# Optimization experiments

Hardware: AMD Instinct MI355X
Metric: run time of the kernel (lower is better)

The kernel has to match this reference:

```python
import jax, jax.numpy as jnp
import numpy as np

B = 131072
OBS = 64
H = 512
LAT = 512
DPC = 32  # dim_per_component -> 16 components of size 32
LN_EPS = 1e-6  # flax nn.LayerNorm default


def _variance_scaling_uniform(key, shape, scale=1.0):
    # variance_scaling(scale, 'fan_avg', 'uniform')
    fan_in, fan_out = shape[0], shape[1]
    fan_avg = (fan_in + fan_out) / 2.0
    limit = np.sqrt(3.0 * scale / fan_avg)
    return jax.random.uniform(key, shape, jnp.float32, -limit, limit)


def setup_inputs() -> dict:
    key = jax.random.key(0)
    ks = jax.random.split(key, 8)
    inp = {
        'observations': jax.random.normal(ks[0], (B, OBS), jnp.float32),
        'goals': jax.random.normal(ks[1], (B, OBS), jnp.float32),
        'W0': _variance_scaling_uniform(ks[2], (OBS, H)),
        'b0': jnp.zeros((H,), jnp.float32),
        'ln0_s': jnp.ones((H,), jnp.float32),
        'ln0_b': jnp.zeros((H,), jnp.float32),
        'W1': _variance_scaling_uniform(ks[3], (H, H)),
        'b1': jnp.zeros((H,), jnp.float32),
        'ln1_s': jnp.ones((H,), jnp.float32),
        'ln1_b': jnp.zeros((H,), jnp.float32),
        'W2': _variance_scaling_uniform(ks[4], (H, H)),
        'b2': jnp.zeros((H,), jnp.float32),
        'ln2_s': jnp.ones((H,), jnp.float32),
        'ln2_b': jnp.zeros((H,), jnp.float32),
        'W3': _variance_scaling_uniform(ks[5], (H, LAT)),
        'b3': jnp.zeros((LAT,), jnp.float32),
        'alpha': jnp.zeros((), jnp.float32),
    }
    return inp


def _layer_norm(x, scale, bias):
    m = x.mean(axis=-1, keepdims=True)
    v = ((x - m) ** 2).mean(axis=-1, keepdims=True)
    return (x - m) / jnp.sqrt(v + LN_EPS) * scale + bias


def _phi(x, W0, b0, ln0_s, ln0_b, W1, b1, ln1_s, ln1_b, W2, b2, ln2_s, ln2_b, W3, b3):
    # LayerNormMLP with activate_final=False: gelu+LN after every layer except last
    x = _layer_norm(jax.nn.gelu(x @ W0 + b0), ln0_s, ln0_b)
    x = _layer_norm(jax.nn.gelu(x @ W1 + b1), ln1_s, ln1_b)
    x = _layer_norm(jax.nn.gelu(x @ W2 + b2), ln2_s, ln2_b)
    return x @ W3 + b3


def _iqe(phi_s, phi_g, alpha):
    # reshape [B, LAT] -> [B, n_components, DPC]
    x = phi_s.reshape(*phi_s.shape[:-1], -1, DPC)
    y = phi_g.reshape(*phi_g.shape[:-1], -1, DPC)
    valid = x < y
    xy = jnp.concatenate(jnp.broadcast_arrays(x, y), axis=-1)  # [B, C, 2*DPC]
    ixy = jnp.argsort(xy, axis=-1)
    sxy = jnp.take_along_axis(xy, ixy, axis=-1)
    neg_inc = jnp.take_along_axis(valid, ixy % DPC, axis=-1) * jnp.where(ixy < DPC, -1, 1)
    neg_inp = jnp.cumsum(neg_inc, axis=-1)
    neg_f = -1.0 * (neg_inp < 0)
    neg_incf = jnp.concatenate([neg_f[..., :1], neg_f[..., 1:] - neg_f[..., :-1]], axis=-1)
    components = (sxy * neg_incf).sum(axis=-1)  # [B, C]
    a = jax.nn.sigmoid(alpha)
    return a * components.mean(axis=-1) + (1.0 - a) * components.max(axis=-1)


def reference(observations, goals, W0, b0, ln0_s, ln0_b, W1, b1, ln1_s, ln1_b,
              W2, b2, ln2_s, ln2_b, W3, b3, alpha):
    params = (W0, b0, ln0_s, ln0_b, W1, b1, ln1_s, ln1_b, W2, b2, ln2_s, ln2_b, W3, b3)
    phi_s = _phi(observations, *params)
    phi_g = _phi(goals, *params)
    return _iqe(phi_s, phi_g, alpha)
```

## Files before the change

### kernel.cpp

```cpp
#include <hip/hip_runtime.h>
#include <hip/hip_bf16.h>
#include <hip/hip_fp16.h>

typedef unsigned short u16;
typedef unsigned int u32;
typedef __attribute__((ext_vector_type(8))) _Float16 f16x8;
typedef __attribute__((ext_vector_type(4))) float f32x4;

#define ROWS 32
#define SSTR 520
#define RSTR 20
#define NEG_INF (-3.0e38f)

__device__ __forceinline__ float bf2f(u16 b) {
  union { u32 u; float f; } c; c.u = ((u32)b) << 16; return c.f;
}
__device__ __forceinline__ u16 f2bf(float f) {
  union { float f; u32 u; } c; c.f = f;
  u32 r = c.u + 0x7FFFu + ((c.u >> 16) & 1u);
  return (u16)(r >> 16);
}
__device__ __forceinline__ float gelu_tanh(float x) {
  float u = 0.7978845608028654f * (x + 0.044715f * x * x * x);
  float e = __expf(2.f * u);
  float t = 1.f - 2.f / (e + 1.f);
  return 0.5f * x * (1.f + t);
}
__device__ __forceinline__ float ldp(const void* p, int i, int f32) {
  return f32 ? ((const float*)p)[i] : bf2f(((const u16*)p)[i]);
}
__device__ __forceinline__ f16x8 load8(const void* base, long off, int f32) {
  f16x8 r;
  if (f32) {
    const float4* p = (const float4*)((const float*)base + off);
    float4 a = p[0], b = p[1];
    r[0] = (_Float16)a.x; r[1] = (_Float16)a.y; r[2] = (_Float16)a.z; r[3] = (_Float16)a.w;
    r[4] = (_Float16)b.x; r[5] = (_Float16)b.y; r[6] = (_Float16)b.z; r[7] = (_Float16)b.w;
  } else {
    const u16* p = (const u16*)base + off;
#pragma unroll
    for (int i = 0; i < 8; ++i) r[i] = (_Float16)bf2f(p[i]);
  }
  return r;
}

__global__ void detect_dtype(const u16* __restrict__ obs, int* flag) {
  int l = threadIdx.x;
  float v = fabsf(bf2f(obs[2 * l]));
  if (v != v) v = 1e30f;
#pragma unroll
  for (int m = 1; m <= 32; m <<= 1) v = fmaxf(v, __shfl_xor(v, m, 64));
  if (l == 0) *flag = (v > 1000.0f) ? 1 : 0;
}

__global__ void pack_frag(const void* __restrict__ src, u16* __restrict__ dst,
                          const int* __restrict__ flag, int total,
                          int fshift, int cishift, int tmask) {
  int id = blockIdx.x * 256 + threadIdx.x;
  if (id >= total) return;
  int j = id & 7;
  int lane = (id >> 3) & 63;
  int fi = id >> 9;
  int w = fi >> fshift;
  int rem = fi & ((1 << fshift) - 1);
  int ci = rem >> cishift;
  int t = rem & tmask;
  int q = lane >> 4, r = lane & 15;
  int ch = w * 64 + ci * 16 + r;
  int k = t * 32 + q * 8 + j;
  float v = ldp(src, k * 512 + ch, *flag);
  dst[id] = __half_as_ushort(__float2half(v));
}

__global__ __launch_bounds__(512, 4) void gciqe_main(
    const void* __restrict__ obs, const void* __restrict__ goals,
    const u16* __restrict__ wT0, const u16* __restrict__ wT1,
    const u16* __restrict__ wT2, const u16* __restrict__ wT3,
    const void* __restrict__ b0, const void* __restrict__ b1,
    const void* __restrict__ b2, const void* __restrict__ b3,
    const void* __restrict__ ls0, const void* __restrict__ lb0,
    const void* __restrict__ ls1, const void* __restrict__ lb1,
    const void* __restrict__ ls2, const void* __restrict__ lb2,
    const void* __restrict__ alphap, void* __restrict__ out,
    const int* __restrict__ flagp)
{
  __shared__ __align__(16) u16 slab[ROWS * SSTR];
  __shared__ __align__(16) float red[ROWS * RSTR];

  const int f32 = *flagp;
  const int tid = threadIdx.x;
  const int lane = tid & 63, w = tid >> 6;
  const int r = lane & 15, q = lane >> 4;
  const int i0 = blockIdx.x * 16;

  f32x4 acc[4][2];

#pragma unroll
  for (int ci = 0; ci < 4; ++ci) {
    acc[ci][0] = (f32x4){0.f, 0.f, 0.f, 0.f};
    acc[ci][1] = (f32x4){0.f, 0.f, 0.f, 0.f};
  }
  {
    f16x8 bf0[2][2];
#pragma unroll
    for (int nt = 0; nt < 2; ++nt) {
      int row = nt * 16 + r;
      const void* base = (row & 1) ? goals : obs;
      long ro = (long)(i0 + (row >> 1)) * 64;
#pragma unroll
      for (int u = 0; u < 2; ++u)
        bf0[nt][u] = load8(base, ro + u * 32 + q * 8, f32);
    }
    const u16* w0base = wT0 + w * 4096;
#pragma unroll
    for (int ci = 0; ci < 4; ++ci) {
#pragma unroll
      for (int u = 0; u < 2; ++u) {
        f16x8 af = *(const f16x8*)(w0base + (ci * 2 + u) * 512 + lane * 8);
        acc[ci][0] = __builtin_amdgcn_mfma_f32_16x16x32_f16(af, bf0[0][u], acc[ci][0], 0, 0, 0);
        acc[ci][1] = __builtin_amdgcn_mfma_f32_16x16x32_f16(af, bf0[1][u], acc[ci][1], 0, 0, 0);
      }
    }
  }

  for (int l = 0; l <= 3; ++l) {
    if (l > 0) {
      const u16* wp = (l == 1) ? wT1 : (l == 2) ? wT2 : wT3;
      const u16* wbase = wp + w * 32768;
#pragma unroll
      for (int ci = 0; ci < 4; ++ci) {
        acc[ci][0] = (f32x4){0.f, 0.f, 0.f, 0.f};
        acc[ci][1] = (f32x4){0.f, 0.f, 0.f, 0.f};
      }
      f16x8 A[2][4];
#pragma unroll
      for (int u = 0; u < 4; ++u)
        A[0][u] = *(const f16x8*)(wbase + u * 512 + lane * 8);
#pragma unroll
      for (int kq = 0; kq < 4; ++kq) {
        f16x8 bfr[2][4];
#pragma unroll
        for (int nt = 0; nt < 2; ++nt)
#pragma unroll
          for (int u = 0; u < 4; ++u)
            bfr[nt][u] = *(const f16x8*)(slab + (nt * 16 + r) * SSTR + kq * 128 + u * 32 + q * 8);
#pragma unroll
        for (int ci = 0; ci < 4; ++ci) {
          const int step = kq * 4 + ci;
          const int cur = step & 1;
          if (step < 15) {
            const int nstep = step + 1;
            const int nci = nstep & 3, nkq = nstep >> 2;
#pragma unroll
            for (int u = 0; u < 4; ++u)
              A[cur ^ 1][u] = *(const f16x8*)(wbase + (nci * 16 + nkq * 4 + u) * 512 + lane * 8);
          }
#pragma unroll
          for (int u = 0; u < 4; ++u) {
            acc[ci][0] = __builtin_amdgcn_mfma_f32_16x16x32_f16(A[cur][u], bfr[0][u], acc[ci][0], 0, 0, 0);
            acc[ci][1] = __builtin_amdgcn_mfma_f32_16x16x32_f16(A[cur][u], bfr[1][u], acc[ci][1], 0, 0, 0);
          }
        }
      }
    }

    if (l < 3) {
      const void* pb  = (l == 0) ? b0 : (l == 1) ? b1 : b2;
      const void* psl = (l == 0) ? ls0 : (l == 1) ? ls1 : ls2;
      const void* plb = (l == 0) ? lb0 : (l == 1) ? lb1 : lb2;
      float bz[4][4];
#pragma unroll
      for (int ci = 0; ci < 4; ++ci) {
        int cb = w * 64 + ci * 16 + q * 4;
#pragma unroll
        for (int j = 0; j < 4; ++j) bz[ci][j] = ldp(pb, cb + j, f32);
      }
      float s[2] = {0.f, 0.f}, t[2] = {0.f, 0.f};
#pragma unroll
      for (int ci = 0; ci < 4; ++ci)
#pragma unroll
        for (int nt = 0; nt < 2; ++nt) {
          f32x4 v = acc[ci][nt];
          v.x = gelu_tanh(v.x + bz[ci][0]); v.y = gelu_tanh(v.y + bz[ci][1]);
          v.z = gelu_tanh(v.z + bz[ci][2]); v.w = gelu_tanh(v.w + bz[ci][3]);
          acc[ci][nt] = v;
          s[nt] += v.x + v.y + v.z + v.w;
          t[nt] += v.x * v.x + v.y * v.y + v.z * v.z + v.w * v.w;
        }
#pragma unroll
      for (int nt = 0; nt < 2; ++nt) {
        s[nt] += __shfl_xor(s[nt], 16, 64); t[nt] += __shfl_xor(t[nt], 16, 64);
        s[nt] += __shfl_xor(s[nt], 32, 64); t[nt] += __shfl_xor(t[nt], 32, 64);
      }
      if (q == 0) {
        *(float2*)(red + (0 * 16 + r) * RSTR + w * 2) = make_float2(s[0], t[0]);
        *(float2*)(red + (1 * 16 + r) * RSTR + w * 2) = make_float2(s[1], t[1]);
      }
      __syncthreads();
      float mean[2], rstd[2];
#pragma unroll
      for (int nt = 0; nt < 2; ++nt) {
        int row = nt * 16 + r;
        float ts = 0.f, tq = 0.f;
#pragma unroll
        for (int p = 0; p < 4; ++p) {
          f32x4 a = *(const f32x4*)(red + row * RSTR + p * 4);
          ts += a.x + a.z; tq += a.y + a.w;
        }
        mean[nt] = ts * (1.f / 512.f);
        rstd[nt] = rsqrtf(tq * (1.f / 512.f) - mean[nt] * mean[nt] + 1e-6f);
      }
      float gs[4][4], gb[4][4];
#pragma unroll
      for (int ci = 0; ci < 4; ++ci) {
        int cb = w * 64 + ci * 16 + q * 4;
#pragma unroll
        for (int j = 0; j < 4; ++j) {
          gs[ci][j] = ldp(psl, cb + j, f32);
          gb[ci][j] = ldp(plb, cb + j, f32);
        }
      }
#pragma unroll
      for (int ci = 0; ci < 4; ++ci) {
        int cb = w * 64 + ci * 16 + q * 4;
#pragma unroll
        for (int nt = 0; nt < 2; ++nt) {
          int row = nt * 16 + r;
          f32x4 v = acc[ci][nt];
          ushort4 o;
          o.x = __half_as_ushort(__float2half((v.x - mean[nt]) * rstd[nt] * gs[ci][0] + gb[ci][0]));
          o.y = __half_as_ushort(__float2half((v.y - mean[nt]) * rstd[nt] * gs[ci][1] + gb[ci][1]));
          o.z = __half_as_ushort(__float2half((v.z - mean[nt]) * rstd[nt] * gs[ci][2] + gb[ci][2]));
          o.w = __half_as_ushort(__float2half((v.w - mean[nt]) * rstd[nt] * gs[ci][3] + gb[ci][3]));
          *(ushort4*)(slab + row * SSTR + cb) = o;
        }
      }
      __syncthreads();
    } else {
#pragma unroll
      for (int ci = 0; ci < 4; ++ci) {
        int cb = w * 64 + ci * 16 + q * 4;
        float bx = ldp(b3, cb + 0, f32), by = ldp(b3, cb + 1, f32);
        float bz2 = ldp(b3, cb + 2, f32), bw = ldp(b3, cb + 3, f32);
#pragma unroll
        for (int nt = 0; nt < 2; ++nt) {
          int row = nt * 16 + r;
          f32x4 v = acc[ci][nt];
          ushort4 o;
          o.x = __half_as_ushort(__float2half(v.x + bx));
          o.y = __half_as_ushort(__float2half(v.y + by));
          o.z = __half_as_ushort(__float2half(v.z + bz2));
          o.w = __half_as_ushort(__float2half(v.w + bw));
          *(ushort4*)(slab + row * SSTR + cb) = o;
        }
      }
      __syncthreads();
    }
  }

  {
    const float al = ldp(alphap, 0, f32);
    const float a = 1.f / (1.f + __expf(-al));
    const int h = lane >> 5, il = lane & 31;
    for (int v = 0; v < 2; ++v) {
      int pL = 2 * w + v;
      float cs = 0.f, cm = 0.f;
      for (int it = 0; it < 8; ++it) {
        int c = 2 * it + h;
        float x = __half2float(__ushort_as_half(slab[(2 * pL) * SSTR + c * 32 + il]));
        float y = __half2float(__ushort_as_half(slab[(2 * pL + 1) * SSTR + c * 32 + il]));
        if (!(x < y)) y = NEG_INF;
#pragma unroll
        for (int k = 2; k <= 32; k <<= 1) {
#pragma unroll
          for (int j = k >> 1; j >= 1; j >>= 1) {
            float xo = __shfl_xor(x, j, 64);
            float yo = __shfl_xor(y, j, 64);
            bool keep_min = (((il & k) == 0) == ((il & j) == 0));
            bool take = keep_min ? (xo < x) : (xo > x);
            if (take) { x = xo; y = yo; }
          }
        }
        float p = __shfl_up(y, 1, 32);
        if (il == 0) p = NEG_INF;
#pragma unroll
        for (int d = 1; d <= 16; d <<= 1) {
          float t2 = __shfl_up(p, d, 32);
          if (il >= d) p = fmaxf(p, t2);
        }
        float contrib = fmaxf(0.f, y - fmaxf(x, p));
#pragma unroll
        for (int msk = 1; msk <= 16; msk <<= 1)
          contrib += __shfl_xor(contrib, msk, 64);
        cs += contrib;
        cm = fmaxf(cm, contrib);
      }
      cs += __shfl_xor(cs, 32, 64);
      cm = fmaxf(cm, __shfl_xor(cm, 32, 64));
      if (lane == 0) {
        float res = a * (cs * (1.f / 16.f)) + (1.f - a) * cm;
        if (f32) ((float*)out)[i0 + pL] = res;
        else ((u16*)out)[i0 + pL] = f2bf(res);
      }
    }
  }
}

extern "C" void kernel_launch(void* const* d_in, const int* in_sizes, int n_in,
                              void* d_out, int out_size, void* d_ws, size_t ws_size,
                              hipStream_t stream) {
  (void)in_sizes; (void)n_in; (void)out_size; (void)ws_size;
  const void* obs   = d_in[0];
  const void* goals = d_in[1];
  const void* W0 = d_in[2];
  const void* b0 = d_in[3];
  const void* ls0 = d_in[4];
  const void* lb0 = d_in[5];
  const void* W1 = d_in[6];
  const void* b1 = d_in[7];
  const void* ls1 = d_in[8];
  const void* lb1 = d_in[9];
  const void* W2 = d_in[10];
  const void* b2 = d_in[11];
  const void* ls2 = d_in[12];
  const void* lb2 = d_in[13];
  const void* W3 = d_in[14];
  const void* b3 = d_in[15];
  const void* alpha = d_in[16];

  int* flag = (int*)d_ws;
  u16* wT0 = (u16*)((char*)d_ws + 64);
  u16* wT1 = wT0 + 512 * 64;
  u16* wT2 = wT1 + 512 * 512;
  u16* wT3 = wT2 + 512 * 512;

  detect_dtype<<<1, 64, 0, stream>>>((const u16*)obs, flag);
  pack_frag<<<128, 256, 0, stream>>>(W0, wT0, flag, 512 * 64, 3, 1, 1);
  pack_frag<<<1024, 256, 0, stream>>>(W1, wT1, flag, 512 * 512, 6, 4, 15);
  pack_frag<<<1024, 256, 0, stream>>>(W2, wT2, flag, 512 * 512, 6, 4, 15);
  pack_frag<<<1024, 256, 0, stream>>>(W3, wT3, flag, 512 * 512, 6, 4, 15);
  gciqe_main<<<8192, 512, 0, stream>>>(obs, goals, wT0, wT1, wT2, wT3,
      b0, b1, b2, b3, ls0, lb0, ls1, lb1, ls2, lb2, alpha, d_out, flag);
}
```

Baseline: 1.143 ms.

## Cut register pressure: drop weight double-buffer, raise occupancy, cheaper gelu and packed converts

```diff
diff --git a/kernel.cpp b/kernel.cpp
--- a/kernel.cpp
+++ b/kernel.cpp
@@ -5,6 +5,7 @@
 typedef unsigned short u16;
 typedef unsigned int u32;
 typedef __attribute__((ext_vector_type(8))) _Float16 f16x8;
+typedef __attribute__((ext_vector_type(2))) __fp16 fp16x2;
 typedef __attribute__((ext_vector_type(4))) float f32x4;
 
 #define ROWS 32
@@ -20,11 +21,18 @@
   u32 r = c.u + 0x7FFFu + ((c.u >> 16) & 1u);
   return (u16)(r >> 16);
 }
+__device__ __forceinline__ u32 pkh(float a, float b) {
+  union { fp16x2 h; u32 u; } c;
+  c.h = __builtin_amdgcn_cvt_pkrtz(a, b);
+  return c.u;
+}
+#define GELU_C1 (-2.302118150990279f)
+#define GELU_C2 (-0.10294019245144983f)
 __device__ __forceinline__ float gelu_tanh(float x) {
-  float u = 0.7978845608028654f * (x + 0.044715f * x * x * x);
-  float e = __expf(2.f * u);
-  float t = 1.f - 2.f / (e + 1.f);
-  return 0.5f * x * (1.f + t);
+  float x2 = x * x;
+  float p = x * __builtin_fmaf(GELU_C2, x2, GELU_C1);
+  float e = __builtin_exp2f(p);
+  return x * __builtin_amdgcn_rcpf(1.f + e);
 }
 __device__ __forceinline__ float ldp(const void* p, int i, int f32) {
   return f32 ? ((const float*)p)[i] : bf2f(((const u16*)p)[i]);
@@ -72,7 +80,7 @@
   dst[id] = __half_as_ushort(__float2half(v));
 }
 
-__global__ __launch_bounds__(512, 4) void gciqe_main(
+__global__ __launch_bounds__(512, 6) void gciqe_main(
     const void* __restrict__ obs, const void* __restrict__ goals,
     const u16* __restrict__ wT0, const u16* __restrict__ wT1,
     const u16* __restrict__ wT2, const u16* __restrict__ wT3,
@@ -132,34 +140,22 @@
         acc[ci][0] = (f32x4){0.f, 0.f, 0.f, 0.f};
         acc[ci][1] = (f32x4){0.f, 0.f, 0.f, 0.f};
       }
-      f16x8 A[2][4];
-#pragma unroll
-      for (int u = 0; u < 4; ++u)
-        A[0][u] = *(const f16x8*)(wbase + u * 512 + lane * 8);
-#pragma unroll
-      for (int kq = 0; kq < 4; ++kq) {
-        f16x8 bfr[2][4];
+#pragma unroll
+      for (int s = 0; s < 8; ++s) {
+        f16x8 bfr[2][2];
 #pragma unroll
         for (int nt = 0; nt < 2; ++nt)
 #pragma unroll
-          for (int u = 0; u < 4; ++u)
-            bfr[nt][u] = *(const f16x8*)(slab + (nt * 16 + r) * SSTR + kq * 128 + u * 32 + q * 8);
+          for (int u = 0; u < 2; ++u)
+            bfr[nt][u] = *(const f16x8*)(slab + (nt * 16 + r) * SSTR + s * 64 + u * 32 + q * 8);
 #pragma unroll
         for (int ci = 0; ci < 4; ++ci) {
-          const int step = kq * 4 + ci;
-          const int cur = step & 1;
-          if (step < 15) {
-            const int nstep = step + 1;
-            const int nci = nstep & 3, nkq = nstep >> 2;
-#pragma unroll
-            for (int u = 0; u < 4; ++u)
-              A[cur ^ 1][u] = *(const f16x8*)(wbase + (nci * 16 + nkq * 4 + u) * 512 + lane * 8);
-          }
-#pragma unroll
-          for (int u = 0; u < 4; ++u) {
-            acc[ci][0] = __builtin_amdgcn_mfma_f32_16x16x32_f16(A[cur][u], bfr[0][u], acc[ci][0], 0, 0, 0);
-            acc[ci][1] = __builtin_amdgcn_mfma_f32_16x16x32_f16(A[cur][u], bfr[1][u], acc[ci][1], 0, 0, 0);
-          }
+          f16x8 A0 = *(const f16x8*)(wbase + (ci * 16 + s * 2 + 0) * 512 + lane * 8);
+          f16x8 A1 = *(const f16x8*)(wbase + (ci * 16 + s * 2 + 1) * 512 + lane * 8);
+          acc[ci][0] = __builtin_amdgcn_mfma_f32_16x16x32_f16(A0, bfr[0][0], acc[ci][0], 0, 0, 0);
+          acc[ci][1] = __builtin_amdgcn_mfma_f32_16x16x32_f16(A0, bfr[1][0], acc[ci][1], 0, 0, 0);
+          acc[ci][0] = __builtin_amdgcn_mfma_f32_16x16x32_f16(A1, bfr[0][1], acc[ci][0], 0, 0, 0);
+          acc[ci][1] = __builtin_amdgcn_mfma_f32_16x16x32_f16(A1, bfr[1][1], acc[ci][1], 0, 0, 0);
         }
       }
     }
@@ -210,29 +206,23 @@
         mean[nt] = ts * (1.f / 512.f);
         rstd[nt] = rsqrtf(tq * (1.f / 512.f) - mean[nt] * mean[nt] + 1e-6f);
       }
-      float gs[4][4], gb[4][4];
 #pragma unroll
       for (int ci = 0; ci < 4; ++ci) {
         int cb = w * 64 + ci * 16 + q * 4;
-#pragma unroll
-        for (int j = 0; j < 4; ++j) {
-          gs[ci][j] = ldp(psl, cb + j, f32);
-          gb[ci][j] = ldp(plb, cb + j, f32);
-        }
-      }
-#pragma unroll
-      for (int ci = 0; ci < 4; ++ci) {
-        int cb = w * 64 + ci * 16 + q * 4;
+        float g0 = ldp(psl, cb + 0, f32), g1 = ldp(psl, cb + 1, f32);
+        float g2 = ldp(psl, cb + 2, f32), g3 = ldp(psl, cb + 3, f32);
+        float o0 = ldp(plb, cb + 0, f32), o1 = ldp(plb, cb + 1, f32);
+        float o2 = ldp(plb, cb + 2, f32), o3 = ldp(plb, cb + 3, f32);
 #pragma unroll
         for (int nt = 0; nt < 2; ++nt) {
           int row = nt * 16 + r;
           f32x4 v = acc[ci][nt];
-          ushort4 o;
-          o.x = __half_as_ushort(__float2half((v.x - mean[nt]) * rstd[nt] * gs[ci][0] + gb[ci][0]));
-          o.y = __half_as_ushort(__float2half((v.y - mean[nt]) * rstd[nt] * gs[ci][1] + gb[ci][1]));
-          o.z = __half_as_ushort(__float2half((v.z - mean[nt]) * rstd[nt] * gs[ci][2] + gb[ci][2]));
-          o.w = __half_as_ushort(__float2half((v.w - mean[nt]) * rstd[nt] * gs[ci][3] + gb[ci][3]));
-          *(ushort4*)(slab + row * SSTR + cb) = o;
+          uint2 o;
+          o.x = pkh((v.x - mean[nt]) * rstd[nt] * g0 + o0,
+                    (v.y - mean[nt]) * rstd[nt] * g1 + o1);
+          o.y = pkh((v.z - mean[nt]) * rstd[nt] * g2 + o2,
+                    (v.w - mean[nt]) * rstd[nt] * g3 + o3);
+          *(uint2*)(slab + row * SSTR + cb) = o;
         }
       }
       __syncthreads();
@@ -246,12 +236,10 @@
         for (int nt = 0; nt < 2; ++nt) {
           int row = nt * 16 + r;
           f32x4 v = acc[ci][nt];
-          ushort4 o;
-          o.x = __half_as_ushort(__float2half(v.x + bx));
-          o.y = __half_as_ushort(__float2half(v.y + by));
-          o.z = __half_as_ushort(__float2half(v.z + bz2));
-          o.w = __half_as_ushort(__float2half(v.w + bw));
-          *(ushort4*)(slab + row * SSTR + cb) = o;
+          uint2 o;
+          o.x = pkh(v.x + bx, v.y + by);
+          o.y = pkh(v.z + bz2, v.w + bw);
+          *(uint2*)(slab + row * SSTR + cb) = o;
         }
       }
       __syncthreads();
@@ -260,7 +248,7 @@
 
   {
     const float al = ldp(alphap, 0, f32);
-    const float a = 1.f / (1.f + __expf(-al));
+    const float a = 1.f / (1.f + __builtin_exp2f(-al * 1.4426950408889634f));
     const int h = lane >> 5, il = lane & 31;
     for (int v = 0; v < 2; ++v) {
       int pL = 2 * w + v;
```

Result: slower. 1.265 ms (+10.7%).
